# Optimization experiments

Measured on AMD Instinct MI355X. Metric: run time of the kernel, lower is better.

Reference implementation:

```python
import jax, jax.numpy as jnp
import numpy as np

M, K, N = 4096, 4096, 11008

def setup_inputs() -> dict:
    key = jax.random.key(0)
    k1, k2, k3, k4, k5 = jax.random.split(key, 5)
    x = jax.random.normal(k1, (M, K), dtype=jnp.float32)
    # int8 weights stored as int32 carrier (values in [-128, 127])
    weight = jax.random.randint(k2, (N, K), -128, 128, dtype=jnp.int32)
    # per-channel dequant scale, small positive values
    deq_scale = jax.random.uniform(k3, (N,), dtype=jnp.float32, minval=1e-4, maxval=2e-3)
    # static per-tensor activation scale
    input_scale = jax.random.uniform(k4, (1,), dtype=jnp.float32, minval=0.02, maxval=0.05)
    input_offset = jnp.zeros((1,), dtype=jnp.int32)
    quant_bias = jax.random.randint(k5, (N,), -1000, 1000, dtype=jnp.int32)
    return {"x": x, "weight": weight, "deq_scale": deq_scale,
            "input_scale": input_scale, "input_offset": input_offset,
            "quant_bias": quant_bias}

def reference(x, weight, deq_scale, input_scale, input_offset, quant_bias):
    # Static per-tensor activation quantization to int8
    x_q = jnp.clip(jnp.round(x / input_scale) + input_offset.astype(jnp.float32),
                   -128.0, 127.0).astype(jnp.int32)  # [M, K]
    # int8 GEMM accumulated in int32 (weight stored [N, K], i.e. transposed)
    acc = jnp.einsum('mk,nk->mn', x_q, weight)  # [M, N] int32
    # add int32 quant bias, per-channel dequant to fp32
    out = (acc + quant_bias[None, :]).astype(jnp.float32) * deq_scale[None, :]
    return out
```

## Files before the change

kernel.cpp:

```cpp
#include <hip/hip_runtime.h>
#include <cstdint>
#include <cstddef>

#define M_DIM 4096
#define K_DIM 4096
#define N_DIM 11008
#define BM 256
#define BN 256
#define BKI 64
#define NT (K_DIM / BKI)
#define NTM (M_DIM / BM)
#define NTN (N_DIM / BN)
#define TILE_A_BYTES (BM * BKI)
#define RING_STRIDE (2 * TILE_A_BYTES)
#define RING 3

typedef int   int4v   __attribute__((ext_vector_type(4)));
typedef float float4v __attribute__((ext_vector_type(4)));

__device__ __forceinline__ void gload_lds16(const void* g, void* l) {
  __builtin_amdgcn_global_load_lds(
      (const __attribute__((address_space(1))) unsigned int*)g,
      (__attribute__((address_space(3))) unsigned int*)l, 16, 0, 0);
}

__global__ void quant_x_kernel(const float* __restrict__ x,
                               const float* __restrict__ scale_p,
                               const int* __restrict__ off_p,
                               signed char* __restrict__ xq, int total16) {
  const float inv = 1.0f / scale_p[0];
  const float off = (float)off_p[0];
  int tid = blockIdx.x * blockDim.x + threadIdx.x;
  int stride = gridDim.x * blockDim.x;
  const float4v* x4 = (const float4v*)x;
  int4v* out4 = (int4v*)xq;
  for (int i = tid; i < total16; i += stride) {
    int4v o;
#pragma unroll
    for (int j = 0; j < 4; ++j) {
      float4v v = x4[(size_t)i * 4 + j];
      int r = 0;
#pragma unroll
      for (int e = 0; e < 4; ++e) {
        float q = rintf(v[e] * inv) + off;
        q = fminf(fmaxf(q, -128.0f), 127.0f);
        int qi = (int)q;
        r |= (qi & 0xff) << (8 * e);
      }
      o[j] = r;
    }
    out4[i] = o;
  }
}

__global__ void pack_w_kernel(const int* __restrict__ w,
                              signed char* __restrict__ wq, int total16) {
  int tid = blockIdx.x * blockDim.x + threadIdx.x;
  int stride = gridDim.x * blockDim.x;
  const int4v* w4 = (const int4v*)w;
  int4v* out4 = (int4v*)wq;
  for (int i = tid; i < total16; i += stride) {
    int4v o;
#pragma unroll
    for (int j = 0; j < 4; ++j) {
      int4v v = w4[(size_t)i * 4 + j];
      o[j] = (v[0] & 0xff) | ((v[1] & 0xff) << 8) |
             ((v[2] & 0xff) << 16) | ((v[3] & 0xff) << 24);
    }
    out4[i] = o;
  }
}

__global__ __launch_bounds__(512, 2) void gemm_i8_kernel(
    const signed char* __restrict__ A,
    const signed char* __restrict__ B,
    const int* __restrict__ qbias,
    const float* __restrict__ dscale,
    float* __restrict__ out) {
  __shared__ __attribute__((aligned(16))) signed char lds[RING * RING_STRIDE];

  const int tid  = threadIdx.x;
  const int lane = tid & 63;
  const int wv   = tid >> 6;
  const int wr   = wv >> 2;
  const int wc   = wv & 3;

  int bid = blockIdx.x;
  int swz = (bid & 7) * ((NTM * NTN) >> 3) + (bid >> 3);
  int tm = swz & (NTM - 1);
  int tn = swz >> 4;

  const signed char* Ab = A + (size_t)tm * BM * K_DIM;
  const signed char* Bb = B + (size_t)tn * BN * K_DIM;

  const int fA    = wv * 2;
  const int srow  = fA * 16 + (lane & 15);
  const int koff  = (lane >> 4) * 16;
  const signed char* gA0 = Ab + (size_t)srow * K_DIM + koff;
  const signed char* gA1 = gA0 + (size_t)16 * K_DIM;
  const signed char* gB0 = Bb + (size_t)srow * K_DIM + koff;
  const signed char* gB1 = gB0 + (size_t)16 * K_DIM;
  const int dstA = fA * 1024;
  const int dstB = TILE_A_BYTES + fA * 1024;

#define STAGE_A(kt, roff) do { \
    gload_lds16(gA0 + (size_t)(kt) * BKI, lds + (roff) + dstA); \
    gload_lds16(gA1 + (size_t)(kt) * BKI, lds + (roff) + dstA + 1024); } while (0)
#define STAGE_B(kt, roff) do { \
    gload_lds16(gB0 + (size_t)(kt) * BKI, lds + (roff) + dstB); \
    gload_lds16(gB1 + (size_t)(kt) * BKI, lds + (roff) + dstB + 1024); } while (0)

  const int rdA = (wr * 8) * 1024 + lane * 16;
  const int rdB = TILE_A_BYTES + (wc * 4) * 1024 + lane * 16;

  int4v acc[8][4];
#pragma unroll
  for (int i = 0; i < 8; ++i)
#pragma unroll
    for (int j = 0; j < 4; ++j) acc[i][j] = (int4v){0, 0, 0, 0};

  STAGE_A(0, 0);
  STAGE_B(0, 0);
  STAGE_A(1, RING_STRIDE);
  STAGE_B(1, RING_STRIDE);
  asm volatile("s_waitcnt vmcnt(4)" ::: "memory");
  __builtin_amdgcn_s_barrier();

  int roff = 0;
  for (int kt = 0; kt < NT; ++kt) {
    int nxt = roff + 2 * RING_STRIDE;
    if (nxt >= RING * RING_STRIDE) nxt -= RING * RING_STRIDE;

    int4v bfr[4], afr[4];
#pragma unroll
    for (int ni = 0; ni < 4; ++ni)
      bfr[ni] = *(const int4v*)(lds + roff + rdB + ni * 1024);
#pragma unroll
    for (int mi = 0; mi < 4; ++mi)
      afr[mi] = *(const int4v*)(lds + roff + rdA + mi * 1024);
    if (kt + 2 < NT) STAGE_A(kt + 2, nxt);
    __builtin_amdgcn_s_barrier();
    asm volatile("s_waitcnt lgkmcnt(0)" ::: "memory");
    __builtin_amdgcn_s_setprio(1);
#pragma unroll
    for (int mi = 0; mi < 4; ++mi)
#pragma unroll
      for (int ni = 0; ni < 4; ++ni)
        acc[mi][ni] = __builtin_amdgcn_mfma_i32_16x16x64_i8(
            afr[mi], bfr[ni], acc[mi][ni], 0, 0, 0);
    __builtin_amdgcn_s_setprio(0);
    __builtin_amdgcn_s_barrier();

#pragma unroll
    for (int mi = 0; mi < 4; ++mi)
      afr[mi] = *(const int4v*)(lds + roff + rdA + (mi + 4) * 1024);
    if (kt + 2 < NT) STAGE_B(kt + 2, nxt);
    __builtin_amdgcn_s_barrier();
    asm volatile("s_waitcnt lgkmcnt(0)" ::: "memory");
    __builtin_amdgcn_s_setprio(1);
#pragma unroll
    for (int mi = 0; mi < 4; ++mi)
#pragma unroll
      for (int ni = 0; ni < 4; ++ni)
        acc[mi + 4][ni] = __builtin_amdgcn_mfma_i32_16x16x64_i8(
            afr[mi], bfr[ni], acc[mi + 4][ni], 0, 0, 0);
    __builtin_amdgcn_s_setprio(0);
    if (kt + 2 < NT) asm volatile("s_waitcnt vmcnt(4)" ::: "memory");
    else             asm volatile("s_waitcnt vmcnt(0)" ::: "memory");
    __builtin_amdgcn_s_barrier();

    roff += RING_STRIDE;
    if (roff >= RING * RING_STRIDE) roff -= RING * RING_STRIDE;
  }
#undef STAGE_A
#undef STAGE_B

  const int col = lane & 15;
  const int rb  = (lane >> 4) * 4;
  const int gm0 = tm * BM + wr * 128;
  const int gn0 = tn * BN + wc * 64;
#pragma unroll
  for (int ni = 0; ni < 4; ++ni) {
    int gn = gn0 + ni * 16 + col;
    float ds = dscale[gn];
    int qb = qbias[gn];
#pragma unroll
    for (int mi = 0; mi < 8; ++mi) {
      int gm = gm0 + mi * 16 + rb;
#pragma unroll
      for (int j = 0; j < 4; ++j)
        out[(size_t)(gm + j) * N_DIM + gn] = (float)(acc[mi][ni][j] + qb) * ds;
    }
  }
}

extern "C" void kernel_launch(void* const* d_in, const int* in_sizes, int n_in,
                              void* d_out, int out_size, void* d_ws, size_t ws_size,
                              hipStream_t stream) {
  const float* x      = (const float*)d_in[0];
  const int*   w      = (const int*)d_in[1];
  const float* dscale = (const float*)d_in[2];
  const float* iscale = (const float*)d_in[3];
  const int*   ioff   = (const int*)d_in[4];
  const int*   qbias  = (const int*)d_in[5];
  float* out = (float*)d_out;

  const size_t xq_bytes = (size_t)M_DIM * K_DIM;
  const size_t wq_bytes = (size_t)N_DIM * K_DIM;
  if (ws_size < xq_bytes + wq_bytes) return;

  signed char* xq = (signed char*)d_ws;
  signed char* wq = (signed char*)d_ws + xq_bytes;

  quant_x_kernel<<<2048, 256, 0, stream>>>(x, iscale, ioff, xq, M_DIM * K_DIM / 16);
  pack_w_kernel<<<2048, 256, 0, stream>>>(w, wq, N_DIM * K_DIM / 16);
  gemm_i8_kernel<<<NTM * NTN, 512, 0, stream>>>(xq, wq, qbias, dscale, out);
}
```

Measured before the change: 288.1 us.

## Halve GEMM M-tile to 128 and merge A/B staging into one phase per k-step

Shrinks the block tile from 256x256 to 128x256 and keeps a three-slot ring of combined A+B tiles. Each thread now issues three unified global-to-LDS loads per k-step, and each step runs a single MFMA phase with one wait and barrier instead of two half-phases. The launch bound now asks for four blocks per CU, and the grid doubles, which aims to improve wave quantization and latency hiding. In exchange, arithmetic intensity drops, so more global traffic is spent on the B operand. The 72KB ring per block also likely limits real residency below the requested four blocks.

New measurement: 351.8 us. 22.1% more time.

```diff
diff --git a/kernel.cpp b/kernel.cpp
--- a/kernel.cpp
+++ b/kernel.cpp
@@ -5,14 +5,15 @@
 #define M_DIM 4096
 #define K_DIM 4096
 #define N_DIM 11008
-#define BM 256
+#define BM 128
 #define BN 256
 #define BKI 64
 #define NT (K_DIM / BKI)
 #define NTM (M_DIM / BM)
 #define NTN (N_DIM / BN)
 #define TILE_A_BYTES (BM * BKI)
-#define RING_STRIDE (2 * TILE_A_BYTES)
+#define TILE_B_BYTES (BN * BKI)
+#define RING_STRIDE (TILE_A_BYTES + TILE_B_BYTES)
 #define RING 3
 
 typedef int   int4v   __attribute__((ext_vector_type(4)));
@@ -71,7 +72,7 @@
   }
 }
 
-__global__ __launch_bounds__(512, 2) void gemm_i8_kernel(
+__global__ __launch_bounds__(512, 4) void gemm_i8_kernel(
     const signed char* __restrict__ A,
     const signed char* __restrict__ B,
     const int* __restrict__ qbias,
@@ -88,42 +89,37 @@
   int bid = blockIdx.x;
   int swz = (bid & 7) * ((NTM * NTN) >> 3) + (bid >> 3);
   int tm = swz & (NTM - 1);
-  int tn = swz >> 4;
-
-  const signed char* Ab = A + (size_t)tm * BM * K_DIM;
-  const signed char* Bb = B + (size_t)tn * BN * K_DIM;
-
-  const int fA    = wv * 2;
-  const int srow  = fA * 16 + (lane & 15);
-  const int koff  = (lane >> 4) * 16;
-  const signed char* gA0 = Ab + (size_t)srow * K_DIM + koff;
-  const signed char* gA1 = gA0 + (size_t)16 * K_DIM;
-  const signed char* gB0 = Bb + (size_t)srow * K_DIM + koff;
-  const signed char* gB1 = gB0 + (size_t)16 * K_DIM;
-  const int dstA = fA * 1024;
-  const int dstB = TILE_A_BYTES + fA * 1024;
-
-#define STAGE_A(kt, roff) do { \
-    gload_lds16(gA0 + (size_t)(kt) * BKI, lds + (roff) + dstA); \
-    gload_lds16(gA1 + (size_t)(kt) * BKI, lds + (roff) + dstA + 1024); } while (0)
-#define STAGE_B(kt, roff) do { \
-    gload_lds16(gB0 + (size_t)(kt) * BKI, lds + (roff) + dstB); \
-    gload_lds16(gB1 + (size_t)(kt) * BKI, lds + (roff) + dstB + 1024); } while (0)
-
-  const int rdA = (wr * 8) * 1024 + lane * 16;
+  int tn = swz >> 5;
+
+  const signed char* gp[3];
+  int lo[3];
+#pragma unroll
+  for (int i = 0; i < 3; ++i) {
+    int f = wv * 3 + i;
+    lo[i] = f * 1024;
+    if (f < 8)
+      gp[i] = A + (size_t)(tm * BM + f * 16 + (lane & 15)) * K_DIM + (lane >> 4) * 16;
+    else
+      gp[i] = B + (size_t)(tn * BN + (f - 8) * 16 + (lane & 15)) * K_DIM + (lane >> 4) * 16;
+  }
+
+#define STAGE(kt, roff) do { \
+    gload_lds16(gp[0] + (size_t)(kt) * BKI, lds + (roff) + lo[0]); \
+    gload_lds16(gp[1] + (size_t)(kt) * BKI, lds + (roff) + lo[1]); \
+    gload_lds16(gp[2] + (size_t)(kt) * BKI, lds + (roff) + lo[2]); } while (0)
+
+  const int rdA = (wr * 4) * 1024 + lane * 16;
   const int rdB = TILE_A_BYTES + (wc * 4) * 1024 + lane * 16;
 
-  int4v acc[8][4];
-#pragma unroll
-  for (int i = 0; i < 8; ++i)
+  int4v acc[4][4];
+#pragma unroll
+  for (int i = 0; i < 4; ++i)
 #pragma unroll
     for (int j = 0; j < 4; ++j) acc[i][j] = (int4v){0, 0, 0, 0};
 
-  STAGE_A(0, 0);
-  STAGE_B(0, 0);
-  STAGE_A(1, RING_STRIDE);
-  STAGE_B(1, RING_STRIDE);
-  asm volatile("s_waitcnt vmcnt(4)" ::: "memory");
+  STAGE(0, 0);
+  STAGE(1, RING_STRIDE);
+  asm volatile("s_waitcnt vmcnt(3)" ::: "memory");
   __builtin_amdgcn_s_barrier();
 
   int roff = 0;
@@ -131,16 +127,16 @@
     int nxt = roff + 2 * RING_STRIDE;
     if (nxt >= RING * RING_STRIDE) nxt -= RING * RING_STRIDE;
 
-    int4v bfr[4], afr[4];
+    int4v afr[4], bfr[4];
+#pragma unroll
+    for (int mi = 0; mi < 4; ++mi)
+      afr[mi] = *(const int4v*)(lds + roff + rdA + mi * 1024);
 #pragma unroll
     for (int ni = 0; ni < 4; ++ni)
       bfr[ni] = *(const int4v*)(lds + roff + rdB + ni * 1024);
-#pragma unroll
-    for (int mi = 0; mi < 4; ++mi)
-      afr[mi] = *(const int4v*)(lds + roff + rdA + mi * 1024);
-    if (kt + 2 < NT) STAGE_A(kt + 2, nxt);
-    __builtin_amdgcn_s_barrier();
-    asm volatile("s_waitcnt lgkmcnt(0)" ::: "memory");
+
+    if (kt + 2 < NT) STAGE(kt + 2, nxt);
+
     __builtin_amdgcn_s_setprio(1);
 #pragma unroll
     for (int mi = 0; mi < 4; ++mi)
@@ -149,35 +145,22 @@
         acc[mi][ni] = __builtin_amdgcn_mfma_i32_16x16x64_i8(
             afr[mi], bfr[ni], acc[mi][ni], 0, 0, 0);
     __builtin_amdgcn_s_setprio(0);
-    __builtin_amdgcn_s_barrier();
-
-#pragma unroll
-    for (int mi = 0; mi < 4; ++mi)
-      afr[mi] = *(const int4v*)(lds + roff + rdA + (mi + 4) * 1024);
-    if (kt + 2 < NT) STAGE_B(kt + 2, nxt);
-    __builtin_amdgcn_s_barrier();
-    asm volatile("s_waitcnt lgkmcnt(0)" ::: "memory");
-    __builtin_amdgcn_s_setprio(1);
-#pragma unroll
-    for (int mi = 0; mi < 4; ++mi)
-#pragma unroll
-      for (int ni = 0; ni < 4; ++ni)
-        acc[mi + 4][ni] = __builtin_amdgcn_mfma_i32_16x16x64_i8(
-            afr[mi], bfr[ni], acc[mi + 4][ni], 0, 0, 0);
-    __builtin_amdgcn_s_setprio(0);
-    if (kt + 2 < NT) asm volatile("s_waitcnt vmcnt(4)" ::: "memory");
-    else             asm volatile("s_waitcnt vmcnt(0)" ::: "memory");
-    __builtin_amdgcn_s_barrier();
-
+
+    if (kt + 2 < NT) {
+      asm volatile("s_waitcnt vmcnt(3)" ::: "memory");
+      __builtin_amdgcn_s_barrier();
+    } else if (kt + 1 < NT) {
+      asm volatile("s_waitcnt vmcnt(0)" ::: "memory");
+      __builtin_amdgcn_s_barrier();
+    }
     roff += RING_STRIDE;
     if (roff >= RING * RING_STRIDE) roff -= RING * RING_STRIDE;
   }
-#undef STAGE_A
-#undef STAGE_B
+#undef STAGE
 
   const int col = lane & 15;
   const int rb  = (lane >> 4) * 4;
-  const int gm0 = tm * BM + wr * 128;
+  const int gm0 = tm * BM + wr * 64;
   const int gn0 = tn * BN + wc * 64;
 #pragma unroll
   for (int ni = 0; ni < 4; ++ni) {
@@ -185,7 +168,7 @@
     float ds = dscale[gn];
     int qb = qbias[gn];
 #pragma unroll
-    for (int mi = 0; mi < 8; ++mi) {
+    for (int mi = 0; mi < 4; ++mi) {
       int gm = gm0 + mi * 16 + rb;
 #pragma unroll
       for (int j = 0; j < 4; ++j)
```
